# Optimization experiments

Measured on AMD Instinct MI355X. Metric: run time of the kernel, lower is better.

## Reference

```python
import jax, jax.numpy as jnp
import numpy as np

DIM = 2048        # config.dim
HID = 1408        # config.moe_inter_dim
E = 16            # config.n_routed_experts
TOPK = 4          # config.n_activated_experts
SHARED = 2816     # n_shared_experts * moe_inter_dim
B, S = 1, 2048
ROUTE_SCALE = 1.0


def setup_inputs() -> dict:
    key = jax.random.key(0)
    ks = jax.random.split(key, 8)
    def w(k, shape, fan_in):
        return jax.random.normal(k, shape, jnp.float32) * (1.0 / np.sqrt(fan_in))
    return {
        "x": jax.random.normal(ks[0], (B, S, DIM), jnp.float32),
        "gate_w": w(ks[1], (E, DIM), DIM),
        "w1": w(ks[2], (E, HID, DIM), DIM),   # per-expert nn.Linear(dim, hid).weight
        "w2": w(ks[3], (E, DIM, HID), HID),   # per-expert nn.Linear(hid, dim).weight
        "w3": w(ks[4], (E, HID, DIM), DIM),
        "sw1": w(ks[5], (SHARED, DIM), DIM),  # shared MLP weights
        "sw2": w(ks[6], (DIM, SHARED), SHARED),
        "sw3": w(ks[7], (SHARED, DIM), DIM),
    }


def reference(x, gate_w, w1, w2, w3, sw1, sw2, sw3):
    shape = x.shape
    xt = x.reshape(-1, DIM)                      # [T, D]
    T = xt.shape[0]

    # --- Gate (score_func='softmax', n_groups=1, bias=None since dim != 7168) ---
    logits = xt @ gate_w.T                        # [T, E]
    scores = jax.nn.softmax(logits.astype(jnp.float32), axis=-1)
    topv, idx = jax.lax.top_k(scores, TOPK)       # n_groups==1: topk over flat scores
    weights = topv * ROUTE_SCALE                  # gather(original_scores, idx) == topv here

    # aux load-balance loss
    tpe = jnp.zeros((E,), jnp.float32).at[idx.reshape(-1)].add(1.0) / (T * TOPK)
    aux_loss = E * jnp.sum(tpe * scores.mean(axis=0))

    # --- Routed experts: combine weights [T, E], then batched SwiGLU GEMMs ---
    comb = jnp.zeros((T, E), jnp.float32).at[jnp.arange(T)[:, None], idx].add(weights)
    h = jax.nn.silu(jnp.einsum('td,ehd->teh', xt, w1)) * jnp.einsum('td,ehd->teh', xt, w3)
    y = jnp.einsum('teh,edh,te->td', h, w2, comb)  # weighted combine (0-weight experts cancel)

    # --- Shared experts (SwiGLU MLP, dropout=0) ---
    z = (jax.nn.silu(xt @ sw1.T) * (xt @ sw3.T)) @ sw2.T

    return (y + z).reshape(shape), aux_loss
```

## Files before the change

kernel.cpp:

```cpp
#include <hip/hip_runtime.h>
#include <hip/hip_bf16.h>

typedef unsigned short u16;
typedef __attribute__((ext_vector_type(8))) short short8;
typedef __attribute__((ext_vector_type(4))) float f32x4;

#define DIM 2048
#define HID 1408
#define NE 16
#define NTOK 2048
#define TOPK_ 4
#define SHID 2816
#define CAPROWS 10240
#define AUX_IDX (2048 * 2048)

__device__ inline u16 f2bf(float f) {
  __bf16 h = (__bf16)f;
  return __builtin_bit_cast(u16, h);
}

__device__ inline void gload_lds16(const void* g, void* l) {
  __builtin_amdgcn_global_load_lds(
      (const __attribute__((address_space(1))) unsigned int*)g,
      (__attribute__((address_space(3))) unsigned int*)l, 16, 0, 0);
}

__global__ __launch_bounds__(256) void gate_dots_kernel(
    const float* __restrict__ x, const float* __restrict__ gw,
    double* __restrict__ logits) {
  int t = blockIdx.x;
  const float* xt = x + (size_t)t * DIM;
  __shared__ double red[NE][4];
  int lane = threadIdx.x & 63, wid = threadIdx.x >> 6;
  for (int e = 0; e < NE; ++e) {
    const float* w = gw + e * DIM;
    double p = 0.0;
    for (int d = threadIdx.x; d < DIM; d += 256)
      p += (double)xt[d] * (double)w[d];
#pragma unroll
    for (int s = 32; s; s >>= 1) p += __shfl_xor(p, s);
    if (lane == 0) red[e][wid] = p;
  }
  __syncthreads();
  if (threadIdx.x < NE) {
    int e = threadIdx.x;
    logits[(size_t)t * NE + e] = red[e][0] + red[e][1] + red[e][2] + red[e][3];
  }
}

__global__ __launch_bounds__(256) void topk_kernel(
    const double* __restrict__ logits,
    int* __restrict__ idxb, float* __restrict__ wtb,
    int* __restrict__ counts, float* __restrict__ ssum) {
  __shared__ int lcnt[NE];
  __shared__ float lsum[NE];
  if (threadIdx.x < NE) { lcnt[threadIdx.x] = 0; lsum[threadIdx.x] = 0.f; }
  __syncthreads();
  int t = blockIdx.x * 256 + threadIdx.x;
  int lane = threadIdx.x & 63;
  double sc[NE];
  double m = -1e300;
#pragma unroll
  for (int e = 0; e < NE; ++e) {
    sc[e] = logits[(size_t)t * NE + e];
    if (sc[e] > m) m = sc[e];
  }
  double s = 0.0;
#pragma unroll
  for (int e = 0; e < NE; ++e) { sc[e] = exp(sc[e] - m); s += sc[e]; }
  double inv = 1.0 / s;
#pragma unroll
  for (int e = 0; e < NE; ++e) sc[e] *= inv;
  unsigned used = 0;
  for (int k = 0; k < TOPK_; ++k) {
    int be = 0; double bv = -1.0;
#pragma unroll
    for (int e = 0; e < NE; ++e)
      if (!((used >> e) & 1u) && sc[e] > bv) { bv = sc[e]; be = e; }
    used |= 1u << be;
    idxb[t * TOPK_ + k] = be;
    wtb[t * TOPK_ + k] = (float)bv;
    atomicAdd(&lcnt[be], 1);
  }
#pragma unroll
  for (int e = 0; e < NE; ++e) {
    float v = (float)sc[e];
#pragma unroll
    for (int sft = 32; sft; sft >>= 1) v += __shfl_xor(v, sft);
    if (lane == 0) atomicAdd(&lsum[e], v);
  }
  __syncthreads();
  if (threadIdx.x < NE) {
    atomicAdd(&counts[threadIdx.x], lcnt[threadIdx.x]);
    atomicAdd(&ssum[threadIdx.x], lsum[threadIdx.x]);
  }
}

__global__ __launch_bounds__(256) void setup_kernel(
    const int* __restrict__ counts, int* __restrict__ off, int* __restrict__ cap,
    const float* __restrict__ ssum, int* __restrict__ perm, float* __restrict__ pwt,
    float* __restrict__ aux_out) {
  if (threadIdx.x == 0) {
    int o = 0; double aux = 0.0;
    for (int e = 0; e < NE; ++e) {
      off[e] = o;
      int c = (counts[e] + 127) & ~127;
      cap[e] = c;
      o += c;
      aux += ((double)counts[e] / (NTOK * TOPK_)) * ((double)ssum[e] / NTOK);
    }
    aux_out[0] = (float)(NE * aux);
  }
  for (int i = threadIdx.x; i < CAPROWS; i += 256) { perm[i] = 0; pwt[i] = 0.f; }
}

__global__ __launch_bounds__(256) void scatter_kernel(
    const int* __restrict__ idxb, const float* __restrict__ wtb,
    const int* __restrict__ off, int* __restrict__ cursor,
    int* __restrict__ perm, float* __restrict__ pwt) {
  int t = blockIdx.x * 256 + threadIdx.x;
  if (t >= NTOK) return;
  for (int k = 0; k < TOPK_; ++k) {
    int e = idxb[t * TOPK_ + k];
    int s = atomicAdd(&cursor[e], 1);
    int p = off[e] + s;
    perm[p] = t;
    pwt[p] = wtb[t * TOPK_ + k];
  }
}

__global__ __launch_bounds__(256) void cvt_kernel(const float* __restrict__ x,
                                                  u16* __restrict__ xb) {
  size_t i = ((size_t)blockIdx.x * 256 + threadIdx.x) * 8;
  float4 a = *(const float4*)(x + i);
  float4 b = *(const float4*)(x + i + 4);
  union { u16 u[8]; uint4 v; } o;
  o.u[0] = f2bf(a.x); o.u[1] = f2bf(a.y); o.u[2] = f2bf(a.z); o.u[3] = f2bf(a.w);
  o.u[4] = f2bf(b.x); o.u[5] = f2bf(b.y); o.u[6] = f2bf(b.z); o.u[7] = f2bf(b.w);
  *(uint4*)(xb + i) = o.v;
}

template <bool GATHER, bool DUAL, int EPI>
__global__ __launch_bounds__(256) void gemm2_kernel(
    const u16* __restrict__ A, int lda,
    const float* __restrict__ B1, const float* __restrict__ B3,
    int ldb, long bstride, int K,
    const int* __restrict__ seg_off, const int* __restrict__ seg_cnt,
    const int* __restrict__ seg_cap,
    const int* __restrict__ perm, const float* __restrict__ pwt,
    float* __restrict__ C0, int ldc0,
    u16* __restrict__ Cb, int ldcb, int Mfixed) {
  int e = blockIdx.z;
  int off = 0, cnt = Mfixed, cap = Mfixed;
  if (seg_off) { off = seg_off[e]; cnt = seg_cnt[e]; cap = seg_cap[e]; }
  if ((int)blockIdx.y * 128 >= cap) return;
  int m0 = off + blockIdx.y * 128;
  int n0 = blockIdx.x * 64;
  const float* Bb1 = B1 + (long)e * bstride;
  const float* Bb3 = DUAL ? (B3 + (long)e * bstride) : nullptr;

  __shared__ u16 As[2][128 * 64];
  __shared__ u16 Bs1[2][64 * 64];
  __shared__ u16 Bs3[DUAL ? 2 * 64 * 64 : 2];

  int tid = threadIdx.x;
  int lane = tid & 63;
  int wid = tid >> 6;
  int wr = wid >> 1, wc = wid & 1;

  f32x4 acc1[4][2], acc3[4][2];
#pragma unroll
  for (int mi = 0; mi < 4; ++mi)
#pragma unroll
    for (int ni = 0; ni < 2; ++ni) {
      acc1[mi][ni] = (f32x4){0.f, 0.f, 0.f, 0.f};
      acc3[mi][ni] = (f32x4){0.f, 0.f, 0.f, 0.f};
    }

  int ar = tid >> 3;
  int ac = (tid & 7) * 8;
  long abase[4];
#pragma unroll
  for (int it = 0; it < 4; ++it) {
    int row = m0 + it * 32 + ar;
    int rid = GATHER ? perm[row] : row;
    abase[it] = (long)rid * lda + ac;
  }
  int brr = tid >> 4;
  int bsl = (tid & 15) * 4;
  long bbase[4];
#pragma unroll
  for (int it = 0; it < 4; ++it)
    bbase[it] = (long)(n0 + it * 16 + brr) * ldb + bsl;

  float4 r1[4], r3[4];

  auto stageA = [&](int buf, int k0) {
#pragma unroll
    for (int it = 0; it < 4; ++it)
      gload_lds16(A + abase[it] + k0, &As[buf][(it * 32 + ar) * 64 + ac]);
  };
  auto loadB = [&](int k0) {
#pragma unroll
    for (int it = 0; it < 4; ++it) r1[it] = *(const float4*)(Bb1 + bbase[it] + k0);
    if (DUAL) {
#pragma unroll
      for (int it = 0; it < 4; ++it) r3[it] = *(const float4*)(Bb3 + bbase[it] + k0);
    }
  };
  auto writeB = [&](int buf) {
#pragma unroll
    for (int it = 0; it < 4; ++it) {
      int lo = (it * 16 + brr) * 64 + bsl;
      ushort4 o;
      o.x = f2bf(r1[it].x); o.y = f2bf(r1[it].y); o.z = f2bf(r1[it].z); o.w = f2bf(r1[it].w);
      *(ushort4*)&Bs1[buf][lo] = o;
      if (DUAL) {
        ushort4 q;
        q.x = f2bf(r3[it].x); q.y = f2bf(r3[it].y); q.z = f2bf(r3[it].z); q.w = f2bf(r3[it].w);
        *(ushort4*)&Bs3[buf * 64 * 64 + lo] = q;
      }
    }
  };

  stageA(0, 0);
  loadB(0);
  writeB(0);
  __syncthreads();

  int NT = K >> 6;
  for (int t = 0; t < NT; ++t) {
    int cur = t & 1, nxt = cur ^ 1;
    bool pf = (t + 1 < NT);
    if (pf) {
      stageA(nxt, (t + 1) << 6);
      loadB((t + 1) << 6);
    }
#pragma unroll
    for (int kk = 0; kk < 64; kk += 32) {
      short8 af[4], b1f[2], b3f[2];
#pragma unroll
      for (int i = 0; i < 4; ++i)
        af[i] = *(const short8*)&As[cur][(wr * 64 + i * 16 + (lane & 15)) * 64 + kk + (lane >> 4) * 8];
#pragma unroll
      for (int i = 0; i < 2; ++i)
        b1f[i] = *(const short8*)&Bs1[cur][(wc * 32 + i * 16 + (lane & 15)) * 64 + kk + (lane >> 4) * 8];
      if (DUAL) {
#pragma unroll
        for (int i = 0; i < 2; ++i)
          b3f[i] = *(const short8*)&Bs3[cur * 64 * 64 + (wc * 32 + i * 16 + (lane & 15)) * 64 + kk + (lane >> 4) * 8];
      }
#pragma unroll
      for (int mi = 0; mi < 4; ++mi)
#pragma unroll
        for (int ni = 0; ni < 2; ++ni) {
          acc1[mi][ni] = __builtin_amdgcn_mfma_f32_16x16x32_bf16(af[mi], b1f[ni], acc1[mi][ni], 0, 0, 0);
          if (DUAL)
            acc3[mi][ni] = __builtin_amdgcn_mfma_f32_16x16x32_bf16(af[mi], b3f[ni], acc3[mi][ni], 0, 0, 0);
        }
    }
    if (pf) writeB(nxt);
    __syncthreads();
  }

  int rbase = m0 + wr * 64 + (lane >> 4) * 4;
  int cbase = n0 + wc * 32 + (lane & 15);
#pragma unroll
  for (int mi = 0; mi < 4; ++mi) {
#pragma unroll
    for (int ni = 0; ni < 2; ++ni) {
      int col = cbase + ni * 16;
#pragma unroll
      for (int r = 0; r < 4; ++r) {
        int row = rbase + mi * 16 + r;
        float v = acc1[mi][ni][r];
        if (EPI == 0) {
          float a3 = acc3[mi][ni][r];
          float sg = v / (1.f + __expf(-v));
          Cb[(long)row * ldcb + col] = f2bf(sg * a3);
        } else if (EPI == 1) {
          C0[(long)row * ldc0 + col] = v;
        } else {
          if (row < off + cnt) {
            atomicAdd(&C0[(long)perm[row] * ldc0 + col], v * pwt[row]);
          }
        }
      }
    }
  }
}

extern "C" void kernel_launch(void* const* d_in, const int* in_sizes, int n_in,
                              void* d_out, int out_size, void* d_ws, size_t ws_size,
                              hipStream_t stream) {
  (void)in_sizes; (void)n_in; (void)out_size; (void)ws_size;
  const float* x   = (const float*)d_in[0];
  const float* gw  = (const float*)d_in[1];
  const float* w1  = (const float*)d_in[2];
  const float* w2  = (const float*)d_in[3];
  const float* w3  = (const float*)d_in[4];
  const float* sw1 = (const float*)d_in[5];
  const float* sw2 = (const float*)d_in[6];
  const float* sw3 = (const float*)d_in[7];
  float* out = (float*)d_out;
  char* ws = (char*)d_ws;

  int*   counts = (int*)(ws + 0);
  int*   cursor = (int*)(ws + 64);
  int*   off    = (int*)(ws + 128);
  int*   cap    = (int*)(ws + 192);
  float* ssum   = (float*)(ws + 256);
  int*   idxb   = (int*)(ws + 4096);
  float* wtb    = (float*)(ws + 4096 + 32768);
  int*   perm   = (int*)(ws + 4096 + 65536);
  float* pwt    = (float*)(ws + 4096 + 65536 + 40960);
  u16*   xb     = (u16*)(ws + 262144);
  double* logits = (double*)(ws + 262144 + 8388608);
  u16*   hbuf   = (u16*)(ws + 262144 + 8388608 + 57671680);
  u16*   hsb    = (u16*)(ws + 262144 + 8388608 + 57671680 + 28835840);

  hipMemsetAsync(ws, 0, 512, stream);
  gate_dots_kernel<<<dim3(NTOK), dim3(256), 0, stream>>>(x, gw, logits);
  topk_kernel<<<dim3(NTOK / 256), dim3(256), 0, stream>>>(logits, idxb, wtb, counts, ssum);
  setup_kernel<<<dim3(1), dim3(256), 0, stream>>>(counts, off, cap, ssum, perm, pwt, out + AUX_IDX);
  scatter_kernel<<<dim3(8), dim3(256), 0, stream>>>(idxb, wtb, off, cursor, perm, pwt);
  cvt_kernel<<<dim3(2048), dim3(256), 0, stream>>>(x, xb);

  gemm2_kernel<true, true, 0><<<dim3(HID / 64, 16, NE), dim3(256), 0, stream>>>(
      xb, DIM, w1, w3, DIM, (long)HID * DIM, DIM, off, counts, cap, perm, pwt,
      nullptr, 0, hbuf, HID, 0);
  gemm2_kernel<false, true, 0><<<dim3(SHID / 64, NTOK / 128, 1), dim3(256), 0, stream>>>(
      xb, DIM, sw1, sw3, DIM, 0, DIM, nullptr, nullptr, nullptr, nullptr, nullptr,
      nullptr, 0, hsb, SHID, NTOK);
  gemm2_kernel<false, false, 1><<<dim3(DIM / 64, NTOK / 128, 1), dim3(256), 0, stream>>>(
      hsb, SHID, sw2, nullptr, SHID, 0, SHID, nullptr, nullptr, nullptr, nullptr, nullptr,
      out, DIM, nullptr, 0, NTOK);
  gemm2_kernel<false, false, 2><<<dim3(DIM / 64, 16, NE), dim3(256), 0, stream>>>(
      hbuf, HID, w2, nullptr, HID, (long)DIM * HID, HID, off, counts, cap, perm, pwt,
      out, DIM, nullptr, 0, 0);
}
```

Before: 713.3 us.

## Use compact tile-to-expert map and M-fastest grid order for grouped GEMMs

The setup kernel now builds a compact list of (expert, row offset) tiles, so the routed GEMMs launch a 1D tile grid instead of a 16x16 grid per expert where most blocks exit early. Grid axes are also swapped so the M tile index is blockIdx.x. Consecutive blocks therefore share the same weight column tile, which should improve L2 reuse of the fp32 weights. The cost is an extra indirection read per block and a serial loop in the single-thread setup kernel.

```diff
diff --git a/kernel.cpp b/kernel.cpp
--- a/kernel.cpp
+++ b/kernel.cpp
@@ -12,6 +12,7 @@
 #define TOPK_ 4
 #define SHID 2816
 #define CAPROWS 10240
+#define MAXTILES (CAPROWS / 128)
 #define AUX_IDX (2048 * 2048)
 
 __device__ inline u16 f2bf(float f) {
@@ -99,16 +100,23 @@
 __global__ __launch_bounds__(256) void setup_kernel(
     const int* __restrict__ counts, int* __restrict__ off, int* __restrict__ cap,
     const float* __restrict__ ssum, int* __restrict__ perm, float* __restrict__ pwt,
-    float* __restrict__ aux_out) {
+    float* __restrict__ aux_out,
+    int* __restrict__ tile2e, int* __restrict__ tile2m0, int* __restrict__ ntiles) {
   if (threadIdx.x == 0) {
-    int o = 0; double aux = 0.0;
+    int o = 0; double aux = 0.0; int nt = 0;
     for (int e = 0; e < NE; ++e) {
       off[e] = o;
       int c = (counts[e] + 127) & ~127;
       cap[e] = c;
+      for (int t = 0; t < (c >> 7); ++t) {
+        tile2e[nt] = e;
+        tile2m0[nt] = o + t * 128;
+        ++nt;
+      }
       o += c;
       aux += ((double)counts[e] / (NTOK * TOPK_)) * ((double)ssum[e] / NTOK);
     }
+    ntiles[0] = nt;
     aux_out[0] = (float)(NE * aux);
   }
   for (int i = threadIdx.x; i < CAPROWS; i += 256) { perm[i] = 0; pwt[i] = 0.f; }
@@ -145,17 +153,25 @@
     const u16* __restrict__ A, int lda,
     const float* __restrict__ B1, const float* __restrict__ B3,
     int ldb, long bstride, int K,
+    const int* __restrict__ tile2e, const int* __restrict__ tile2m0,
+    const int* __restrict__ ntiles,
     const int* __restrict__ seg_off, const int* __restrict__ seg_cnt,
-    const int* __restrict__ seg_cap,
     const int* __restrict__ perm, const float* __restrict__ pwt,
     float* __restrict__ C0, int ldc0,
     u16* __restrict__ Cb, int ldcb, int Mfixed) {
-  int e = blockIdx.z;
-  int off = 0, cnt = Mfixed, cap = Mfixed;
-  if (seg_off) { off = seg_off[e]; cnt = seg_cnt[e]; cap = seg_cap[e]; }
-  if ((int)blockIdx.y * 128 >= cap) return;
-  int m0 = off + blockIdx.y * 128;
-  int n0 = blockIdx.x * 64;
+  int e, m0, rowlim;
+  if (tile2e) {
+    if ((int)blockIdx.x >= ntiles[0]) return;
+    e = tile2e[blockIdx.x];
+    m0 = tile2m0[blockIdx.x];
+    rowlim = seg_off[e] + seg_cnt[e];
+  } else {
+    e = 0;
+    m0 = blockIdx.x * 128;
+    if (m0 >= Mfixed) return;
+    rowlim = Mfixed;
+  }
+  int n0 = blockIdx.y * 64;
   const float* Bb1 = B1 + (long)e * bstride;
   const float* Bb3 = DUAL ? (B3 + (long)e * bstride) : nullptr;
 
@@ -281,7 +297,7 @@
         } else if (EPI == 1) {
           C0[(long)row * ldc0 + col] = v;
         } else {
-          if (row < off + cnt) {
+          if (row < rowlim) {
             atomicAdd(&C0[(long)perm[row] * ldc0 + col], v * pwt[row]);
           }
         }
@@ -310,6 +326,9 @@
   int*   off    = (int*)(ws + 128);
   int*   cap    = (int*)(ws + 192);
   float* ssum   = (float*)(ws + 256);
+  int*   ntiles = (int*)(ws + 512);
+  int*   tile2e = (int*)(ws + 1024);
+  int*   tile2m0= (int*)(ws + 2048);
   int*   idxb   = (int*)(ws + 4096);
   float* wtb    = (float*)(ws + 4096 + 32768);
   int*   perm   = (int*)(ws + 4096 + 65536);
@@ -322,20 +341,21 @@
   hipMemsetAsync(ws, 0, 512, stream);
   gate_dots_kernel<<<dim3(NTOK), dim3(256), 0, stream>>>(x, gw, logits);
   topk_kernel<<<dim3(NTOK / 256), dim3(256), 0, stream>>>(logits, idxb, wtb, counts, ssum);
-  setup_kernel<<<dim3(1), dim3(256), 0, stream>>>(counts, off, cap, ssum, perm, pwt, out + AUX_IDX);
+  setup_kernel<<<dim3(1), dim3(256), 0, stream>>>(counts, off, cap, ssum, perm, pwt,
+                                                  out + AUX_IDX, tile2e, tile2m0, ntiles);
   scatter_kernel<<<dim3(8), dim3(256), 0, stream>>>(idxb, wtb, off, cursor, perm, pwt);
   cvt_kernel<<<dim3(2048), dim3(256), 0, stream>>>(x, xb);
 
-  gemm2_kernel<true, true, 0><<<dim3(HID / 64, 16, NE), dim3(256), 0, stream>>>(
-      xb, DIM, w1, w3, DIM, (long)HID * DIM, DIM, off, counts, cap, perm, pwt,
-      nullptr, 0, hbuf, HID, 0);
-  gemm2_kernel<false, true, 0><<<dim3(SHID / 64, NTOK / 128, 1), dim3(256), 0, stream>>>(
-      xb, DIM, sw1, sw3, DIM, 0, DIM, nullptr, nullptr, nullptr, nullptr, nullptr,
-      nullptr, 0, hsb, SHID, NTOK);
-  gemm2_kernel<false, false, 1><<<dim3(DIM / 64, NTOK / 128, 1), dim3(256), 0, stream>>>(
-      hsb, SHID, sw2, nullptr, SHID, 0, SHID, nullptr, nullptr, nullptr, nullptr, nullptr,
-      out, DIM, nullptr, 0, NTOK);
-  gemm2_kernel<false, false, 2><<<dim3(DIM / 64, 16, NE), dim3(256), 0, stream>>>(
-      hbuf, HID, w2, nullptr, HID, (long)DIM * HID, HID, off, counts, cap, perm, pwt,
-      out, DIM, nullptr, 0, 0);
-}
+  gemm2_kernel<true, true, 0><<<dim3(MAXTILES, HID / 64, 1), dim3(256), 0, stream>>>(
+      xb, DIM, w1, w3, DIM, (long)HID * DIM, DIM, tile2e, tile2m0, ntiles,
+      off, counts, perm, pwt, nullptr, 0, hbuf, HID, 0);
+  gemm2_kernel<false, true, 0><<<dim3(NTOK / 128, SHID / 64, 1), dim3(256), 0, stream>>>(
+      xb, DIM, sw1, sw3, DIM, 0, DIM, nullptr, nullptr, nullptr,
+      nullptr, nullptr, nullptr, nullptr, nullptr, 0, hsb, SHID, NTOK);
+  gemm2_kernel<false, false, 1><<<dim3(NTOK / 128, DIM / 64, 1), dim3(256), 0, stream>>>(
+      hsb, SHID, sw2, nullptr, SHID, 0, SHID, nullptr, nullptr, nullptr,
+      nullptr, nullptr, nullptr, nullptr, out, DIM, nullptr, 0, NTOK);
+  gemm2_kernel<false, false, 2><<<dim3(MAXTILES, DIM / 64, 1), dim3(256), 0, stream>>>(
+      hbuf, HID, w2, nullptr, HID, (long)DIM * HID, HID, tile2e, tile2m0, ntiles,
+      off, counts, perm, pwt, out, DIM, nullptr, 0, 0);
+}
```

Result: slower. 762.1 us (+6.8%).

## Merge routed and shared expert GEMMs into two combined launches with compacted tile slots

Applied to the files above, without the earlier changes.

Setup now builds a compacted list of (expert, row-tile) slots, interleaved across the grid. Routed and shared GEMMs for each phase run in one launch, so empty expert tiles no longer cost launched blocks and the shared work fills the GPU alongside the routed work. The shared down-projection now accumulates into the output with atomics, which requires an added memset of the output. In exchange there are more atomics on the output and runtime branching inside the kernel.

```diff
diff --git a/kernel.cpp b/kernel.cpp
--- a/kernel.cpp
+++ b/kernel.cpp
@@ -12,6 +12,7 @@
 #define TOPK_ 4
 #define SHID 2816
 #define CAPROWS 10240
+#define NSLOT 96
 #define AUX_IDX (2048 * 2048)
 
 __device__ inline u16 f2bf(float f) {
@@ -99,13 +100,22 @@
 __global__ __launch_bounds__(256) void setup_kernel(
     const int* __restrict__ counts, int* __restrict__ off, int* __restrict__ cap,
     const float* __restrict__ ssum, int* __restrict__ perm, float* __restrict__ pwt,
-    float* __restrict__ aux_out) {
+    float* __restrict__ aux_out,
+    int* __restrict__ rE, int* __restrict__ rM0) {
+  for (int i = threadIdx.x; i < NSLOT; i += 256) rE[i] = -1;
+  __syncthreads();
   if (threadIdx.x == 0) {
-    int o = 0; double aux = 0.0;
+    int o = 0; double aux = 0.0; int nt = 0;
     for (int e = 0; e < NE; ++e) {
       off[e] = o;
       int c = (counts[e] + 127) & ~127;
       cap[e] = c;
+      for (int t = 0; t < (c >> 7); ++t) {
+        int slot = (nt / 12) + (nt % 12) * 8;
+        rE[slot] = e;
+        rM0[slot] = o + t * 128;
+        ++nt;
+      }
       o += c;
       aux += ((double)counts[e] / (NTOK * TOPK_)) * ((double)ssum[e] / NTOK);
     }
@@ -129,39 +139,72 @@
   }
 }
 
-__global__ __launch_bounds__(256) void cvt_kernel(const float* __restrict__ x,
-                                                  u16* __restrict__ xb) {
-  size_t i = ((size_t)blockIdx.x * 256 + threadIdx.x) * 8;
-  float4 a = *(const float4*)(x + i);
-  float4 b = *(const float4*)(x + i + 4);
-  union { u16 u[8]; uint4 v; } o;
-  o.u[0] = f2bf(a.x); o.u[1] = f2bf(a.y); o.u[2] = f2bf(a.z); o.u[3] = f2bf(a.w);
-  o.u[4] = f2bf(b.x); o.u[5] = f2bf(b.y); o.u[6] = f2bf(b.z); o.u[7] = f2bf(b.w);
-  *(uint4*)(xb + i) = o.v;
-}
-
-template <bool GATHER, bool DUAL, int EPI>
-__global__ __launch_bounds__(256) void gemm2_kernel(
-    const u16* __restrict__ A, int lda,
-    const float* __restrict__ B1, const float* __restrict__ B3,
-    int ldb, long bstride, int K,
+__global__ __launch_bounds__(256) void cvtN_kernel(const float* __restrict__ in,
+                                                   u16* __restrict__ out, long n) {
+  long stride = (long)gridDim.x * 2048;
+  for (long i = ((long)blockIdx.x * 256 + threadIdx.x) * 8; i < n; i += stride) {
+    float4 a = *(const float4*)(in + i);
+    float4 b = *(const float4*)(in + i + 4);
+    union { u16 u[8]; uint4 v; } o;
+    o.u[0] = f2bf(a.x); o.u[1] = f2bf(a.y); o.u[2] = f2bf(a.z); o.u[3] = f2bf(a.w);
+    o.u[4] = f2bf(b.x); o.u[5] = f2bf(b.y); o.u[6] = f2bf(b.z); o.u[7] = f2bf(b.w);
+    *(uint4*)(out + i) = o.v;
+  }
+}
+
+template <int PHASE>
+__global__ __launch_bounds__(256) void mgemm_kernel(
+    const u16* __restrict__ xb,
+    const u16* __restrict__ hbuf, const u16* __restrict__ hsb,
+    const float* __restrict__ WrA, const float* __restrict__ WrB,
+    const float* __restrict__ WsA, const float* __restrict__ WsB,
+    float* __restrict__ out,
+    const int* __restrict__ rE, const int* __restrict__ rM0,
     const int* __restrict__ seg_off, const int* __restrict__ seg_cnt,
-    const int* __restrict__ seg_cap,
-    const int* __restrict__ perm, const float* __restrict__ pwt,
-    float* __restrict__ C0, int ldc0,
-    u16* __restrict__ Cb, int ldcb, int Mfixed) {
-  int e = blockIdx.z;
-  int off = 0, cnt = Mfixed, cap = Mfixed;
-  if (seg_off) { off = seg_off[e]; cnt = seg_cnt[e]; cap = seg_cap[e]; }
-  if ((int)blockIdx.y * 128 >= cap) return;
-  int m0 = off + blockIdx.y * 128;
-  int n0 = blockIdx.x * 64;
-  const float* Bb1 = B1 + (long)e * bstride;
-  const float* Bb3 = DUAL ? (B3 + (long)e * bstride) : nullptr;
+    const int* __restrict__ perm, const float* __restrict__ pwt) {
+  constexpr bool DUAL = (PHASE == 1);
+  int x = blockIdx.x, y = blockIdx.y;
+  bool routed = (x < NSLOT);
+  const u16* A; const float *B1, *B3 = nullptr; u16* Cb = nullptr;
+  int lda, K, n0, m0, ldc, rowlim = 0;
+  bool gather = false;
+  if (routed) {
+    int e = rE[x];
+    if (e < 0) return;
+    m0 = rM0[x];
+    if (PHASE == 1) {
+      if (y >= HID / 64) return;
+      A = xb; lda = DIM; K = DIM; gather = true;
+      B1 = WrA + (long)e * HID * DIM;
+      B3 = WrB + (long)e * HID * DIM;
+      n0 = y * 64; Cb = (u16*)hbuf; ldc = HID;
+    } else {
+      A = hbuf; lda = HID; K = HID;
+      B1 = WrA + (long)e * DIM * HID;
+      n0 = y * 64; ldc = DIM;
+      rowlim = seg_off[e] + seg_cnt[e];
+    }
+  } else {
+    if (PHASE == 1) {
+      int j = (x - NSLOT) >> 1, sub = x & 1;
+      m0 = j * 128;
+      A = xb; lda = DIM; K = DIM;
+      B1 = WsA; B3 = WsB;
+      n0 = (y + sub * 22) * 64;
+      Cb = (u16*)hsb; ldc = SHID;
+    } else {
+      int j = x - NSLOT;
+      m0 = j * 128;
+      A = hsb; lda = SHID; K = SHID;
+      B1 = WsA;
+      n0 = y * 64; ldc = DIM;
+    }
+  }
+  int ldb = K;
 
   __shared__ u16 As[2][128 * 64];
   __shared__ u16 Bs1[2][64 * 64];
-  __shared__ u16 Bs3[DUAL ? 2 * 64 * 64 : 2];
+  __shared__ u16 Bs3[DUAL ? 2 : 1][DUAL ? 64 * 64 : 1];
 
   int tid = threadIdx.x;
   int lane = tid & 63;
@@ -183,7 +226,7 @@
 #pragma unroll
   for (int it = 0; it < 4; ++it) {
     int row = m0 + it * 32 + ar;
-    int rid = GATHER ? perm[row] : row;
+    int rid = gather ? perm[row] : row;
     abase[it] = (long)rid * lda + ac;
   }
   int brr = tid >> 4;
@@ -202,10 +245,10 @@
   };
   auto loadB = [&](int k0) {
 #pragma unroll
-    for (int it = 0; it < 4; ++it) r1[it] = *(const float4*)(Bb1 + bbase[it] + k0);
+    for (int it = 0; it < 4; ++it) r1[it] = *(const float4*)(B1 + bbase[it] + k0);
     if (DUAL) {
 #pragma unroll
-      for (int it = 0; it < 4; ++it) r3[it] = *(const float4*)(Bb3 + bbase[it] + k0);
+      for (int it = 0; it < 4; ++it) r3[it] = *(const float4*)(B3 + bbase[it] + k0);
     }
   };
   auto writeB = [&](int buf) {
@@ -218,13 +261,13 @@
       if (DUAL) {
         ushort4 q;
         q.x = f2bf(r3[it].x); q.y = f2bf(r3[it].y); q.z = f2bf(r3[it].z); q.w = f2bf(r3[it].w);
-        *(ushort4*)&Bs3[buf * 64 * 64 + lo] = q;
+        *(ushort4*)&Bs3[buf][lo] = q;
       }
     }
   };
 
+  loadB(0);
   stageA(0, 0);
-  loadB(0);
   writeB(0);
   __syncthreads();
 
@@ -248,7 +291,7 @@
       if (DUAL) {
 #pragma unroll
         for (int i = 0; i < 2; ++i)
-          b3f[i] = *(const short8*)&Bs3[cur * 64 * 64 + (wc * 32 + i * 16 + (lane & 15)) * 64 + kk + (lane >> 4) * 8];
+          b3f[i] = *(const short8*)&Bs3[cur][(wc * 32 + i * 16 + (lane & 15)) * 64 + kk + (lane >> 4) * 8];
       }
 #pragma unroll
       for (int mi = 0; mi < 4; ++mi)
@@ -274,15 +317,16 @@
       for (int r = 0; r < 4; ++r) {
         int row = rbase + mi * 16 + r;
         float v = acc1[mi][ni][r];
-        if (EPI == 0) {
+        if (PHASE == 1) {
           float a3 = acc3[mi][ni][r];
           float sg = v / (1.f + __expf(-v));
-          Cb[(long)row * ldcb + col] = f2bf(sg * a3);
-        } else if (EPI == 1) {
-          C0[(long)row * ldc0 + col] = v;
+          Cb[(long)row * ldc + col] = f2bf(sg * a3);
         } else {
-          if (row < off + cnt) {
-            atomicAdd(&C0[(long)perm[row] * ldc0 + col], v * pwt[row]);
+          if (routed) {
+            if (row < rowlim)
+              atomicAdd(&out[(long)perm[row] * DIM + col], v * pwt[row]);
+          } else {
+            atomicAdd(&out[(long)row * DIM + col], v);
           }
         }
       }
@@ -310,32 +354,28 @@
   int*   off    = (int*)(ws + 128);
   int*   cap    = (int*)(ws + 192);
   float* ssum   = (float*)(ws + 256);
+  int*   rE     = (int*)(ws + 1024);
+  int*   rM0    = (int*)(ws + 2048);
   int*   idxb   = (int*)(ws + 4096);
   float* wtb    = (float*)(ws + 4096 + 32768);
   int*   perm   = (int*)(ws + 4096 + 65536);
   float* pwt    = (float*)(ws + 4096 + 65536 + 40960);
   u16*   xb     = (u16*)(ws + 262144);
-  double* logits = (double*)(ws + 262144 + 8388608);
-  u16*   hbuf   = (u16*)(ws + 262144 + 8388608 + 57671680);
-  u16*   hsb    = (u16*)(ws + 262144 + 8388608 + 57671680 + 28835840);
+  double* logits = (double*)(ws + 8650752);
+  u16*   hbuf   = (u16*)(ws + 16777216);
+  u16*   hsb    = (u16*)(ws + 45613056);
 
   hipMemsetAsync(ws, 0, 512, stream);
+  hipMemsetAsync(out, 0, (size_t)NTOK * DIM * sizeof(float), stream);
   gate_dots_kernel<<<dim3(NTOK), dim3(256), 0, stream>>>(x, gw, logits);
   topk_kernel<<<dim3(NTOK / 256), dim3(256), 0, stream>>>(logits, idxb, wtb, counts, ssum);
-  setup_kernel<<<dim3(1), dim3(256), 0, stream>>>(counts, off, cap, ssum, perm, pwt, out + AUX_IDX);
+  setup_kernel<<<dim3(1), dim3(256), 0, stream>>>(counts, off, cap, ssum, perm, pwt,
+                                                  out + AUX_IDX, rE, rM0);
   scatter_kernel<<<dim3(8), dim3(256), 0, stream>>>(idxb, wtb, off, cursor, perm, pwt);
-  cvt_kernel<<<dim3(2048), dim3(256), 0, stream>>>(x, xb);
-
-  gemm2_kernel<true, true, 0><<<dim3(HID / 64, 16, NE), dim3(256), 0, stream>>>(
-      xb, DIM, w1, w3, DIM, (long)HID * DIM, DIM, off, counts, cap, perm, pwt,
-      nullptr, 0, hbuf, HID, 0);
-  gemm2_kernel<false, true, 0><<<dim3(SHID / 64, NTOK / 128, 1), dim3(256), 0, stream>>>(
-      xb, DIM, sw1, sw3, DIM, 0, DIM, nullptr, nullptr, nullptr, nullptr, nullptr,
-      nullptr, 0, hsb, SHID, NTOK);
-  gemm2_kernel<false, false, 1><<<dim3(DIM / 64, NTOK / 128, 1), dim3(256), 0, stream>>>(
-      hsb, SHID, sw2, nullptr, SHID, 0, SHID, nullptr, nullptr, nullptr, nullptr, nullptr,
-      out, DIM, nullptr, 0, NTOK);
-  gemm2_kernel<false, false, 2><<<dim3(DIM / 64, 16, NE), dim3(256), 0, stream>>>(
-      hbuf, HID, w2, nullptr, HID, (long)DIM * HID, HID, off, counts, cap, perm, pwt,
-      out, DIM, nullptr, 0, 0);
-}
+  cvtN_kernel<<<dim3(2048), dim3(256), 0, stream>>>(x, xb, (long)NTOK * DIM);
+
+  mgemm_kernel<1><<<dim3(NSLOT + 32, HID / 64), dim3(256), 0, stream>>>(
+      xb, hbuf, hsb, w1, w3, sw1, sw3, out, rE, rM0, off, counts, perm, pwt);
+  mgemm_kernel<2><<<dim3(NSLOT + 16, DIM / 64), dim3(256), 0, stream>>>(
+      xb, hbuf, hsb, w2, nullptr, sw2, nullptr, out, rE, rM0, off, counts, perm, pwt);
+}
```

New measurement: 912.8 us. +28.0%, slower.
